# Performance work log

Measured on AMD Instinct MI355X. Metric: run time of the kernel, lower is better.

Reference implementation:

```python
import jax, jax.numpy as jnp
import numpy as np

B, N, E, EA = 4, 100000, 160000, 80000
HID, ED = 128, 16

def _xavier(key, fan_in, fan_out):
    lim = float(np.sqrt(6.0 / (fan_in + fan_out)))
    return jax.random.uniform(key, (fan_in, fan_out), jnp.float32, -lim, lim)

def setup_inputs() -> dict:
    key = jax.random.key(0)
    k1, k2, k3, k4, k5, k6 = jax.random.split(key, 6)
    h = jax.random.normal(k1, (B, N, HID), jnp.float32)
    edge_index = jax.random.randint(k2, (2, E), 0, N, jnp.int64)
    edge_attr = jax.random.normal(k3, (B, E, ED), jnp.float32)
    # index-array equivalent of the boolean edge_type_mask (even count EA)
    edge_type_idx = jnp.sort(jax.random.randint(k4, (EA,), 0, E, jnp.int64))
    d_in = 2 * HID + ED
    W1 = _xavier(k5, d_in, HID)
    b1 = jnp.zeros((HID,), jnp.float32)
    W2 = _xavier(k6, HID, 2)
    b2 = jnp.zeros((2,), jnp.float32)
    return {"h": h, "edge_index": edge_index, "edge_attr": edge_attr,
            "edge_type_idx": edge_type_idx, "W1": W1, "b1": b1, "W2": W2, "b2": b2}

def reference(h, edge_index, edge_attr, edge_type_idx, W1, b1, W2, b2):
    # gather only the masked edges (same math as gather-all then mask)
    sel_r = edge_index[0][edge_type_idx]   # [EA]
    sel_s = edge_index[1][edge_type_idx]   # [EA]
    h_received_a = h[:, sel_r, :]          # [B, EA, HID]
    h_sent_a = h[:, sel_s, :]              # [B, EA, HID]
    edge_attr_a = edge_attr[:, edge_type_idx, :]  # [B, EA, ED]
    x = jnp.concatenate([h_received_a, h_sent_a, edge_attr_a], axis=-1)
    x = jax.nn.relu(jnp.einsum('bef,fh->beh', x, W1) + b1)
    out = jnp.einsum('beh,ho->beo', x, W2) + b2      # [B, EA, 2]
    b, ea, o = out.shape
    return out.reshape(b, ea // 2, 2, o).mean(axis=2)  # [B, EA//2, 2]
```

## Files before the change

### kernel.cpp

```cpp
#include <hip/hip_runtime.h>

#define NB 4
#define N_NODES 100000
#define E_EDGES 160000
#define EA_E 80000
#define HID 128
#define ED 16

#define TILE_M 128
#define THREADS 256
#define XPAD 40
#define WPAD 40

typedef __attribute__((ext_vector_type(8))) short bf16x8;
typedef __attribute__((ext_vector_type(4))) float f32x4;
typedef __attribute__((ext_vector_type(8))) unsigned short u16x8;
typedef __attribute__((ext_vector_type(4))) unsigned short u16x4;

__device__ __forceinline__ unsigned short f2bf(float f) {
    union { float f; unsigned u; } v; v.f = f;
    return (unsigned short)((v.u + 0x7fffu + ((v.u >> 16) & 1u)) >> 16);
}

__global__ __launch_bounds__(THREADS, 3) void actor_head_mfma(
    const float* __restrict__ h,
    const int*   __restrict__ edge_index,
    const float* __restrict__ edge_attr,
    const int*   __restrict__ etype,
    const float* __restrict__ W1,
    const float* __restrict__ b1,
    const float* __restrict__ W2,
    const float* __restrict__ b2,
    float*       __restrict__ out)
{
    __shared__ unsigned short xs[TILE_M][XPAD];
    __shared__ unsigned short ws[HID][WPAD];
    __shared__ int sel[3][TILE_M];

    const int b  = blockIdx.y;
    const int e0 = blockIdx.x * TILE_M;
    const int t  = threadIdx.x;

    if (t < TILE_M) {
        int ei = etype[e0 + t];
        sel[2][t] = ei;
        sel[0][t] = edge_index[ei];
        sel[1][t] = edge_index[E_EDGES + ei];
    }

    const int lane = t & 63;
    const int wid  = t >> 6;
    const int wm   = wid * 32;
    const int fr   = lane & 15;
    const int fq   = lane >> 4;

    const int sm = t >> 1;
    const int sh = t & 1;
    const int kb = t >> 5;
    const int nb = t & 31;

    f32x4 acc[2][8];
    #pragma unroll
    for (int i = 0; i < 2; ++i)
        #pragma unroll
        for (int j = 0; j < 8; ++j) acc[i][j] = (f32x4){0.f, 0.f, 0.f, 0.f};

    __syncthreads();

    for (int c = 0; c < 9; ++c) {
        {
            unsigned short tmp[16];
            if (c < 8) {
                const int node = (c < 4) ? sel[0][sm] : sel[1][sm];
                const float* src = h + ((size_t)b * N_NODES + node) * HID
                                     + (c & 3) * 32 + sh * 16;
                #pragma unroll
                for (int j = 0; j < 4; ++j) {
                    f32x4 v = *reinterpret_cast<const f32x4*>(src + j * 4);
                    tmp[j * 4 + 0] = f2bf(v[0]);
                    tmp[j * 4 + 1] = f2bf(v[1]);
                    tmp[j * 4 + 2] = f2bf(v[2]);
                    tmp[j * 4 + 3] = f2bf(v[3]);
                }
            } else if (sh == 0) {
                const float* src = edge_attr + ((size_t)b * E_EDGES + sel[2][sm]) * ED;
                #pragma unroll
                for (int j = 0; j < 4; ++j) {
                    f32x4 v = *reinterpret_cast<const f32x4*>(src + j * 4);
                    tmp[j * 4 + 0] = f2bf(v[0]);
                    tmp[j * 4 + 1] = f2bf(v[1]);
                    tmp[j * 4 + 2] = f2bf(v[2]);
                    tmp[j * 4 + 3] = f2bf(v[3]);
                }
            } else {
                #pragma unroll
                for (int j = 0; j < 16; ++j) tmp[j] = 0;
            }
            u16x8 lo, hi;
            #pragma unroll
            for (int j = 0; j < 8; ++j) { lo[j] = tmp[j]; hi[j] = tmp[8 + j]; }
            *reinterpret_cast<u16x8*>(&xs[sm][sh * 16 + 0]) = lo;
            *reinterpret_cast<u16x8*>(&xs[sm][sh * 16 + 8]) = hi;
        }

        {
            const int k0 = kb * 4;
            const int n0 = nb * 4;
            float vals[4][4];
            const bool valid = (c < 8) || (k0 < 16);
            if (valid) {
                #pragma unroll
                for (int i = 0; i < 4; ++i) {
                    f32x4 v = *reinterpret_cast<const f32x4*>(
                        W1 + (size_t)(c * 32 + k0 + i) * HID + n0);
                    vals[i][0] = v[0]; vals[i][1] = v[1];
                    vals[i][2] = v[2]; vals[i][3] = v[3];
                }
            } else {
                #pragma unroll
                for (int i = 0; i < 4; ++i)
                    #pragma unroll
                    for (int j = 0; j < 4; ++j) vals[i][j] = 0.f;
            }
            #pragma unroll
            for (int j = 0; j < 4; ++j) {
                u16x4 w;
                w[0] = f2bf(vals[0][j]); w[1] = f2bf(vals[1][j]);
                w[2] = f2bf(vals[2][j]); w[3] = f2bf(vals[3][j]);
                *reinterpret_cast<u16x4*>(&ws[n0 + j][k0]) = w;
            }
        }
        __syncthreads();

        {
            bf16x8 af[2], bw[8];
            #pragma unroll
            for (int mi = 0; mi < 2; ++mi)
                af[mi] = *reinterpret_cast<const bf16x8*>(&xs[wm + mi * 16 + fr][fq * 8]);
            #pragma unroll
            for (int ni = 0; ni < 8; ++ni)
                bw[ni] = *reinterpret_cast<const bf16x8*>(&ws[ni * 16 + fr][fq * 8]);
            #pragma unroll
            for (int mi = 0; mi < 2; ++mi)
                #pragma unroll
                for (int ni = 0; ni < 8; ++ni)
                    acc[mi][ni] = __builtin_amdgcn_mfma_f32_16x16x32_bf16(
                        af[mi], bw[ni], acc[mi][ni], 0, 0, 0);
        }
        __syncthreads();
    }

    float b1v[8], w2a[8], w2b[8];
    #pragma unroll
    for (int ni = 0; ni < 8; ++ni) {
        int n = ni * 16 + fr;
        b1v[ni] = b1[n];
        w2a[ni] = W2[2 * n + 0];
        w2b[ni] = W2[2 * n + 1];
    }
    const float b20 = b2[0], b21 = b2[1];

    #pragma unroll
    for (int mi = 0; mi < 2; ++mi) {
        #pragma unroll
        for (int j = 0; j < 2; ++j) {
            float s0 = 0.f, s1 = 0.f;
            #pragma unroll
            for (int ni = 0; ni < 8; ++ni) {
                float y0 = fmaxf(acc[mi][ni][2 * j]     + b1v[ni], 0.f);
                float y1 = fmaxf(acc[mi][ni][2 * j + 1] + b1v[ni], 0.f);
                float ys = y0 + y1;
                s0 = fmaf(ys, w2a[ni], s0);
                s1 = fmaf(ys, w2b[ni], s1);
            }
            #pragma unroll
            for (int off = 8; off >= 1; off >>= 1) {
                s0 += __shfl_xor(s0, off);
                s1 += __shfl_xor(s1, off);
            }
            if (fr == 0) {
                int mg = e0 + wm + mi * 16 + fq * 4 + 2 * j;
                size_t oi = ((size_t)b * (EA_E / 2) + (mg >> 1)) * 2;
                out[oi + 0] = 0.5f * s0 + b20;
                out[oi + 1] = 0.5f * s1 + b21;
            }
        }
    }
}

extern "C" void kernel_launch(void* const* d_in, const int* in_sizes, int n_in,
                              void* d_out, int out_size, void* d_ws, size_t ws_size,
                              hipStream_t stream) {
    const float* h          = (const float*)d_in[0];
    const int*   edge_index = (const int*)d_in[1];
    const float* edge_attr  = (const float*)d_in[2];
    const int*   etype      = (const int*)d_in[3];
    const float* W1         = (const float*)d_in[4];
    const float* b1         = (const float*)d_in[5];
    const float* W2         = (const float*)d_in[6];
    const float* b2         = (const float*)d_in[7];
    float* out = (float*)d_out;

    dim3 grid(EA_E / TILE_M, NB);
    actor_head_mfma<<<grid, THREADS, 0, stream>>>(
        h, edge_index, edge_attr, etype, W1, b1, W2, b2, out);
}
```

Before: 67.83 us.

## Pre-pack W1 into MFMA fragment layout and prefetch next gather chunk into registers

A small prep kernel converts W1 to bf16 in per-lane MFMA B-fragment order every call, so the main kernel reads weight fragments straight from global/L2 instead of converting and staging them through shared memory. The h/edge_attr gather for the next K-chunk is issued into registers before the current chunk's MFMAs, overlapping gather latency with compute. Launch bounds are raised to 4 blocks per SM, and the float-to-bf16 conversion now uses the HIP intrinsic. This adds a second launch and keeps more data live in registers.

```diff
diff --git a/kernel.cpp b/kernel.cpp
--- a/kernel.cpp
+++ b/kernel.cpp
@@ -1,4 +1,5 @@
 #include <hip/hip_runtime.h>
+#include <hip/hip_bf16.h>
 
 #define NB 4
 #define N_NODES 100000
@@ -10,31 +11,47 @@
 #define TILE_M 128
 #define THREADS 256
 #define XPAD 40
-#define WPAD 40
 
 typedef __attribute__((ext_vector_type(8))) short bf16x8;
 typedef __attribute__((ext_vector_type(4))) float f32x4;
 typedef __attribute__((ext_vector_type(8))) unsigned short u16x8;
-typedef __attribute__((ext_vector_type(4))) unsigned short u16x4;
 
 __device__ __forceinline__ unsigned short f2bf(float f) {
-    union { float f; unsigned u; } v; v.f = f;
-    return (unsigned short)((v.u + 0x7fffu + ((v.u >> 16) & 1u)) >> 16);
-}
-
-__global__ __launch_bounds__(THREADS, 3) void actor_head_mfma(
+    __hip_bfloat16 b = __float2bfloat16(f);
+    union { __hip_bfloat16 b; unsigned short u; } v; v.b = b;
+    return v.u;
+}
+
+__global__ void prep_w1(const float* __restrict__ W1, unsigned short* __restrict__ W1F) {
+    const int cb   = blockIdx.x;
+    const int c    = cb >> 3;
+    const int ni   = cb & 7;
+    const int lane = threadIdx.x;
+    const int fr   = lane & 15;
+    const int fq   = lane >> 4;
+    const int n    = ni * 16 + fr;
+    u16x8 v;
+    #pragma unroll
+    for (int j = 0; j < 8; ++j) {
+        int k = c * 32 + fq * 8 + j;
+        float f = (k < 272) ? W1[(size_t)k * HID + n] : 0.f;
+        v[j] = f2bf(f);
+    }
+    *reinterpret_cast<u16x8*>(W1F + ((size_t)(cb * 64 + lane)) * 8) = v;
+}
+
+__global__ __launch_bounds__(THREADS, 4) void actor_head_mfma(
     const float* __restrict__ h,
     const int*   __restrict__ edge_index,
     const float* __restrict__ edge_attr,
     const int*   __restrict__ etype,
-    const float* __restrict__ W1,
+    const unsigned short* __restrict__ W1F,
     const float* __restrict__ b1,
     const float* __restrict__ W2,
     const float* __restrict__ b2,
     float*       __restrict__ out)
 {
     __shared__ unsigned short xs[TILE_M][XPAD];
-    __shared__ unsigned short ws[HID][WPAD];
     __shared__ int sel[3][TILE_M];
 
     const int b  = blockIdx.y;
@@ -56,8 +73,8 @@
 
     const int sm = t >> 1;
     const int sh = t & 1;
-    const int kb = t >> 5;
-    const int nb = t & 31;
+
+    f32x4 tv[4];
 
     f32x4 acc[2][8];
     #pragma unroll
@@ -67,85 +84,60 @@
 
     __syncthreads();
 
+    {
+        const int node = sel[0][sm];
+        const float* src = h + ((size_t)b * N_NODES + node) * HID + sh * 16;
+        #pragma unroll
+        for (int j = 0; j < 4; ++j) tv[j] = *reinterpret_cast<const f32x4*>(src + j * 4);
+    }
+
     for (int c = 0; c < 9; ++c) {
         {
-            unsigned short tmp[16];
-            if (c < 8) {
-                const int node = (c < 4) ? sel[0][sm] : sel[1][sm];
+            u16x8 lo, hi;
+            #pragma unroll
+            for (int j = 0; j < 4; ++j) {
+                lo[j]     = f2bf(tv[0][j]);
+                lo[4 + j] = f2bf(tv[1][j]);
+                hi[j]     = f2bf(tv[2][j]);
+                hi[4 + j] = f2bf(tv[3][j]);
+            }
+            *reinterpret_cast<u16x8*>(&xs[sm][sh * 16 + 0]) = lo;
+            *reinterpret_cast<u16x8*>(&xs[sm][sh * 16 + 8]) = hi;
+        }
+        __syncthreads();
+
+        if (c < 8) {
+            const int cn = c + 1;
+            if (cn < 8) {
+                const int node = (cn < 4) ? sel[0][sm] : sel[1][sm];
                 const float* src = h + ((size_t)b * N_NODES + node) * HID
-                                     + (c & 3) * 32 + sh * 16;
-                #pragma unroll
-                for (int j = 0; j < 4; ++j) {
-                    f32x4 v = *reinterpret_cast<const f32x4*>(src + j * 4);
-                    tmp[j * 4 + 0] = f2bf(v[0]);
-                    tmp[j * 4 + 1] = f2bf(v[1]);
-                    tmp[j * 4 + 2] = f2bf(v[2]);
-                    tmp[j * 4 + 3] = f2bf(v[3]);
-                }
+                                     + (cn & 3) * 32 + sh * 16;
+                #pragma unroll
+                for (int j = 0; j < 4; ++j) tv[j] = *reinterpret_cast<const f32x4*>(src + j * 4);
             } else if (sh == 0) {
                 const float* src = edge_attr + ((size_t)b * E_EDGES + sel[2][sm]) * ED;
                 #pragma unroll
-                for (int j = 0; j < 4; ++j) {
-                    f32x4 v = *reinterpret_cast<const f32x4*>(src + j * 4);
-                    tmp[j * 4 + 0] = f2bf(v[0]);
-                    tmp[j * 4 + 1] = f2bf(v[1]);
-                    tmp[j * 4 + 2] = f2bf(v[2]);
-                    tmp[j * 4 + 3] = f2bf(v[3]);
-                }
+                for (int j = 0; j < 4; ++j) tv[j] = *reinterpret_cast<const f32x4*>(src + j * 4);
             } else {
                 #pragma unroll
-                for (int j = 0; j < 16; ++j) tmp[j] = 0;
-            }
-            u16x8 lo, hi;
-            #pragma unroll
-            for (int j = 0; j < 8; ++j) { lo[j] = tmp[j]; hi[j] = tmp[8 + j]; }
-            *reinterpret_cast<u16x8*>(&xs[sm][sh * 16 + 0]) = lo;
-            *reinterpret_cast<u16x8*>(&xs[sm][sh * 16 + 8]) = hi;
+                for (int j = 0; j < 4; ++j) tv[j] = (f32x4){0.f, 0.f, 0.f, 0.f};
+            }
         }
 
         {
-            const int k0 = kb * 4;
-            const int n0 = nb * 4;
-            float vals[4][4];
-            const bool valid = (c < 8) || (k0 < 16);
-            if (valid) {
-                #pragma unroll
-                for (int i = 0; i < 4; ++i) {
-                    f32x4 v = *reinterpret_cast<const f32x4*>(
-                        W1 + (size_t)(c * 32 + k0 + i) * HID + n0);
-                    vals[i][0] = v[0]; vals[i][1] = v[1];
-                    vals[i][2] = v[2]; vals[i][3] = v[3];
-                }
-            } else {
-                #pragma unroll
-                for (int i = 0; i < 4; ++i)
-                    #pragma unroll
-                    for (int j = 0; j < 4; ++j) vals[i][j] = 0.f;
-            }
-            #pragma unroll
-            for (int j = 0; j < 4; ++j) {
-                u16x4 w;
-                w[0] = f2bf(vals[0][j]); w[1] = f2bf(vals[1][j]);
-                w[2] = f2bf(vals[2][j]); w[3] = f2bf(vals[3][j]);
-                *reinterpret_cast<u16x4*>(&ws[n0 + j][k0]) = w;
-            }
-        }
-        __syncthreads();
-
-        {
-            bf16x8 af[2], bw[8];
+            bf16x8 af[2];
             #pragma unroll
             for (int mi = 0; mi < 2; ++mi)
                 af[mi] = *reinterpret_cast<const bf16x8*>(&xs[wm + mi * 16 + fr][fq * 8]);
             #pragma unroll
-            for (int ni = 0; ni < 8; ++ni)
-                bw[ni] = *reinterpret_cast<const bf16x8*>(&ws[ni * 16 + fr][fq * 8]);
-            #pragma unroll
-            for (int mi = 0; mi < 2; ++mi)
-                #pragma unroll
-                for (int ni = 0; ni < 8; ++ni)
+            for (int ni = 0; ni < 8; ++ni) {
+                bf16x8 bw = *reinterpret_cast<const bf16x8*>(
+                    W1F + ((size_t)((c * 8 + ni) * 64 + lane)) * 8);
+                #pragma unroll
+                for (int mi = 0; mi < 2; ++mi)
                     acc[mi][ni] = __builtin_amdgcn_mfma_f32_16x16x32_bf16(
-                        af[mi], bw[ni], acc[mi][ni], 0, 0, 0);
+                        af[mi], bw, acc[mi][ni], 0, 0, 0);
+            }
         }
         __syncthreads();
     }
@@ -201,7 +193,11 @@
     const float* b2         = (const float*)d_in[7];
     float* out = (float*)d_out;
 
+    unsigned short* W1F = (unsigned short*)d_ws;
+
+    prep_w1<<<72, 64, 0, stream>>>(W1, W1F);
+
     dim3 grid(EA_E / TILE_M, NB);
     actor_head_mfma<<<grid, THREADS, 0, stream>>>(
-        h, edge_index, edge_attr, etype, W1, b1, W2, b2, out);
-}
+        h, edge_index, edge_attr, etype, W1F, b1, W2, b2, out);
+}
```

Result: slower. 87.31 us (+28.7%).
